# Optimization experiments

Hardware: AMD Instinct MI355X
Metric: run time of the kernel (lower is better)

The kernel has to match this reference:

```python
import jax, jax.numpy as jnp
import numpy as np

ODIM = 8192      # output dim (slice target)
MSIZE = 64       # tile size
N_BLOCKS = 1024  # size of shared block bank


def setup_inputs() -> dict:
    key = jax.random.key(0)
    k1, k2, k3, k4 = jax.random.split(key, 4)
    x = jax.random.normal(k1, (256, 8192), dtype=jnp.float32)
    # bank of msize x msize module blocks (scaled like fan-in init)
    blocks = jax.random.normal(k2, (N_BLOCKS, MSIZE, MSIZE), dtype=jnp.float32) * 0.02
    bound = 1.0 / np.sqrt(ODIM).astype(np.float32)
    bias = jax.random.uniform(k3, (ODIM,), dtype=jnp.float32, minval=-bound, maxval=bound)
    # parts: [icount, ocount] indices into the block bank
    parts = jax.random.randint(k4, (128, 128), 0, N_BLOCKS)
    return {"x": x, "blocks": blocks, "bias": bias, "parts": parts}


def reference(x, blocks, bias, parts):
    icount, ocount = parts.shape
    m = blocks.shape[-1]
    # build_mosaic: gather blocks per parts and tile into a dense weight matrix
    fc = blocks[parts]                                   # [ic, oc, m, m]
    fc_mat = fc.transpose(0, 2, 1, 3).reshape(icount * m, ocount * m)
    # idim (8192) is divisible by msize, so pad is identity (rem == 0 branch)
    y = x @ fc_mat                                       # [B, oc*m]
    y = y[..., :ODIM] + bias                             # slice + bias; post = Identity
    return y
```

## Files before the change

kernel.cpp:

```cpp
#include <hip/hip_runtime.h>
#include <stdint.h>

#define BATCH 256
#define IDIM  8192
#define ODIM  8192
#define MS    64
#define IC    128
#define OC    128
#define NB    1024

#define TM 128
#define TN 128
#define KSPLIT 4
#define NIB (IC / KSPLIT)

#define A_BASE(s) ((s) * 8192)
#define B_BASE(s) (16384 + (s) * 8192)

typedef __bf16 bf16x8 __attribute__((ext_vector_type(8)));
typedef float  floatx4 __attribute__((ext_vector_type(4)));

#define WAITCNT_VM(n) ((((n) & 15) | (((n) >> 4) << 14)) | 0x70 | 0xF00)

__device__ __forceinline__ void async_load16(unsigned short* lds_p, const unsigned short* g_p) {
    __builtin_amdgcn_global_load_lds(
        (const __attribute__((address_space(1))) unsigned int*)g_p,
        (__attribute__((address_space(3))) unsigned int*)lds_p,
        16, 0, 0);
}

__device__ __forceinline__ unsigned short f32_to_bf16(float f) {
    unsigned int u = __float_as_uint(f);
    u += 0x7FFFu + ((u >> 16) & 1u);
    return (unsigned short)(u >> 16);
}

#define XCONV_BLKS 1024
#define PT_BLKS 64
__global__ void k_convert(const float* __restrict__ x, const float* __restrict__ blocks,
                          const int* __restrict__ parts,
                          unsigned short* __restrict__ xb, unsigned short* __restrict__ bt,
                          int* __restrict__ pT) {
    __shared__ float tile[MS][MS + 1];
    int b = blockIdx.x;
    if (b < NB) {
        const float4* src4 = (const float4*)(blocks + (size_t)b * MS * MS);
        unsigned short* dst = bt + (size_t)b * MS * MS;
        #pragma unroll
        for (int i = 0; i < 4; ++i) {
            int slot = i * 256 + threadIdx.x;
            int r = slot >> 4, c4 = (slot & 15) * 4;
            float4 v = src4[slot];
            tile[r][c4 + 0] = v.x; tile[r][c4 + 1] = v.y;
            tile[r][c4 + 2] = v.z; tile[r][c4 + 3] = v.w;
        }
        __syncthreads();
        #pragma unroll
        for (int i = 0; i < 2; ++i) {
            int slot = i * 256 + threadIdx.x;
            int c = slot >> 3, o = slot & 7;
            union { unsigned short s[8]; uint4 v; } u;
            #pragma unroll
            for (int j = 0; j < 8; ++j) u.s[j] = f32_to_bf16(tile[o * 8 + j][c]);
            *(uint4*)(dst + c * MS + o * 8) = u.v;
        }
    } else if (b < NB + XCONV_BLKS) {
        int t = (b - NB) * 256 + threadIdx.x;
        const float4* x4 = (const float4*)x;
        float4 a = x4[2 * t], bb = x4[2 * t + 1];
        union { unsigned short s[8]; uint4 v; } u;
        u.s[0] = f32_to_bf16(a.x);  u.s[1] = f32_to_bf16(a.y);
        u.s[2] = f32_to_bf16(a.z);  u.s[3] = f32_to_bf16(a.w);
        u.s[4] = f32_to_bf16(bb.x); u.s[5] = f32_to_bf16(bb.y);
        u.s[6] = f32_to_bf16(bb.z); u.s[7] = f32_to_bf16(bb.w);
        ((uint4*)xb)[t] = u.v;
    } else {
        int t = (b - NB - XCONV_BLKS) * 256 + threadIdx.x;
        int oc = t >> 7, ic = t & 127;
        pT[t] = parts[ic * OC + oc];
    }
}

extern __shared__ unsigned short smem[];

__global__ __launch_bounds__(256, 2)
void k_mosaic_gemm(const unsigned short* __restrict__ xb,
                   const unsigned short* __restrict__ bt,
                   const int* __restrict__ pT,
                   float* __restrict__ partial) {
    const int tid  = threadIdx.x;
    const int lane = tid & 63;
    const int wave = tid >> 6;
    const int wrow = wave >> 1;
    const int wcol = wave & 1;
    const int nt = blockIdx.x;
    const int mt = blockIdx.y;
    const int ks = blockIdx.z;

    const int m0  = mt * TM;
    const int ob0 = nt * 2;
    const int ib0 = ks * NIB;

    const int row  = lane & 15;
    const int quad = lane >> 4;

    int pv0 = pT[ob0 * IC + ib0 + (lane & 31)];
    int pv1 = pT[(ob0 + 1) * IC + ib0 + (lane & 31)];

    int a_off[2][4], b_off[2][4];
    #pragma unroll
    for (int kk = 0; kk < 2; ++kk) {
        int oct = kk * 4 + quad;
        #pragma unroll
        for (int mi = 0; mi < 4; ++mi) {
            int r = wrow * 64 + mi * 16 + row;
            a_off[kk][mi] = r * MS + ((oct ^ (r & 7)) << 3);
        }
        #pragma unroll
        for (int ni = 0; ni < 4; ++ni) {
            int n = wcol * 64 + ni * 16 + row;
            b_off[kk][ni] = n * MS + ((oct ^ (n & 7)) << 3);
        }
    }

    floatx4 acc[4][4];
    #pragma unroll
    for (int mi = 0; mi < 4; ++mi)
        #pragma unroll
        for (int ni = 0; ni < 4; ++ni)
            acc[mi][ni] = (floatx4){0.f, 0.f, 0.f, 0.f};

#define STAGE_A(abase, ibx) do {                                              \
    _Pragma("unroll")                                                         \
    for (int j = 0; j < 4; ++j) {                                             \
        int slot = j * 256 + tid;               \
        int m = slot >> 3;                                                    \
        int oct = (slot & 7) ^ (m & 7);                                       \
        async_load16(smem + (abase) + slot * 8,                               \
                     xb + (size_t)(m0 + m) * IDIM + (ibx) * MS + oct * 8);    \
    } } while (0)

#define STAGE_B(bbase, pa, pb) do {                                           \
    _Pragma("unroll")                                                         \
    for (int j = 0; j < 4; ++j) {                                             \
        int slot = j * 256 + tid;               \
        int n = slot >> 3;                                                    \
        int oct = (slot & 7) ^ (n & 7);                                       \
        int p = (j < 2) ? (pa) : (pb);                                        \
        async_load16(smem + (bbase) + slot * 8,                               \
                     bt + (size_t)p * (MS * MS) + (n & 63) * MS + oct * 8);   \
    } } while (0)

#define COMPUTE(abase, bbase) do {                                            \
    _Pragma("unroll")                                                         \
    for (int kk = 0; kk < 2; ++kk) {                                          \
        bf16x8 af[4], bfr[4];                                                 \
        _Pragma("unroll")                                                     \
        for (int mi = 0; mi < 4; ++mi)                                        \
            af[mi] = *(const bf16x8*)(smem + (abase) + a_off[kk][mi]);        \
        _Pragma("unroll")                                                     \
        for (int ni = 0; ni < 4; ++ni)                                        \
            bfr[ni] = *(const bf16x8*)(smem + (bbase) + b_off[kk][ni]);       \
        _Pragma("unroll")                                                     \
        for (int mi = 0; mi < 4; ++mi)                                        \
            _Pragma("unroll")                                                 \
            for (int ni = 0; ni < 4; ++ni)                                    \
                acc[mi][ni] = __builtin_amdgcn_mfma_f32_16x16x32_bf16(        \
                    af[mi], bfr[ni], acc[mi][ni], 0, 0, 0);                   \
    } } while (0)

#define ROUND(idx, acS, bcS, asS, bsS) do {                                   \
    STAGE_A(A_BASE(asS), ib0 + (idx) + 1);                                    \
    { int q0 = __shfl(pv0, (idx) + 2), q1 = __shfl(pv1, (idx) + 2);           \
      STAGE_B(B_BASE(bsS), q0, q1); }                                         \
    __builtin_amdgcn_sched_barrier(0);                                        \
    __builtin_amdgcn_s_waitcnt(WAITCNT_VM(12));                               \
    __builtin_amdgcn_s_barrier();                                             \
    __builtin_amdgcn_sched_barrier(0);                                        \
    COMPUTE(A_BASE(acS), B_BASE(bcS));                                        \
    __builtin_amdgcn_sched_barrier(0);                                        \
    __builtin_amdgcn_s_barrier();                                             \
    __builtin_amdgcn_sched_barrier(0);                                        \
    } while (0)

    STAGE_A(A_BASE(0), ib0 + 0);
    { int q0 = __shfl(pv0, 0), q1 = __shfl(pv1, 0); STAGE_B(B_BASE(0), q0, q1); }
    { int q0 = __shfl(pv0, 1), q1 = __shfl(pv1, 1); STAGE_B(B_BASE(1), q0, q1); }

    for (int i6 = 0; i6 < 30; i6 += 6) {
        ROUND(i6 + 0, 0, 0, 1, 2);
        ROUND(i6 + 1, 1, 1, 0, 0);
        ROUND(i6 + 2, 0, 2, 1, 1);
        ROUND(i6 + 3, 1, 0, 0, 2);
        ROUND(i6 + 4, 0, 1, 1, 0);
        ROUND(i6 + 5, 1, 2, 0, 1);
    }
    STAGE_A(A_BASE(1), ib0 + NIB - 1);
    __builtin_amdgcn_sched_barrier(0);
    __builtin_amdgcn_s_waitcnt(WAITCNT_VM(8));
    __builtin_amdgcn_s_barrier();
    __builtin_amdgcn_sched_barrier(0);
    COMPUTE(A_BASE(0), B_BASE(0));
    __builtin_amdgcn_sched_barrier(0);
    __builtin_amdgcn_s_barrier();
    __builtin_amdgcn_sched_barrier(0);
    __builtin_amdgcn_s_waitcnt(WAITCNT_VM(0));
    __builtin_amdgcn_s_barrier();
    __builtin_amdgcn_sched_barrier(0);
    COMPUTE(A_BASE(1), B_BASE(1));

    float* out = partial + (size_t)ks * BATCH * ODIM;
    #pragma unroll
    for (int mi = 0; mi < 4; ++mi)
        #pragma unroll
        for (int ni = 0; ni < 4; ++ni)
            #pragma unroll
            for (int r = 0; r < 4; ++r) {
                int rowg = m0 + wrow * 64 + mi * 16 + quad * 4 + r;
                int colg = nt * TN + wcol * 64 + ni * 16 + row;
                out[(size_t)rowg * ODIM + colg] = acc[mi][ni][r];
            }
}

__global__ void k_reduce_bias(const float* __restrict__ partial,
                              const float* __restrict__ bias,
                              float* __restrict__ out) {
    int t = blockIdx.x * 256 + threadIdx.x;
    const float4* b4 = (const float4*)bias;
    float4 c = b4[t & (ODIM / 4 - 1)];
    float4 r = {c.x, c.y, c.z, c.w};
    #pragma unroll
    for (int k = 0; k < KSPLIT; ++k) {
        const float4* p = (const float4*)(partial + (size_t)k * BATCH * ODIM);
        float4 a = p[t];
        r.x += a.x; r.y += a.y; r.z += a.z; r.w += a.w;
    }
    ((float4*)out)[t] = r;
}

extern "C" void kernel_launch(void* const* d_in, const int* in_sizes, int n_in,
                              void* d_out, int out_size, void* d_ws, size_t ws_size,
                              hipStream_t stream) {
    const float* x      = (const float*)d_in[0];
    const float* blocks = (const float*)d_in[1];
    const float* bias   = (const float*)d_in[2];
    const int*   parts  = (const int*)d_in[3];
    float* out = (float*)d_out;

    char* ws = (char*)d_ws;
    unsigned short* xb      = (unsigned short*)ws;
    unsigned short* btb     = (unsigned short*)(ws + (4u << 20));
    int*            pTr     = (int*)(ws + (12u << 20));
    float*          partial = (float*)(ws + (13u << 20));

    static bool attr_set = false;
    if (!attr_set) {
        hipFuncSetAttribute((const void*)k_mosaic_gemm,
                            hipFuncAttributeMaxDynamicSharedMemorySize, 80 * 1024);
        attr_set = true;
    }

    k_convert<<<NB + XCONV_BLKS + PT_BLKS, 256, 0, stream>>>(x, blocks, parts, xb, btb, pTr);
    k_mosaic_gemm<<<dim3(ODIM / TN, BATCH / TM, KSPLIT), 256, 80 * 1024, stream>>>(xb, btb, pTr, partial);
    k_reduce_bias<<<(BATCH * ODIM) / (256 * 4), 256, 0, stream>>>(partial, bias, out);
}
```

Before: 121.4 us.

## Load A fragments directly from global into double-buffered registers, drop A LDS staging

The A (activation) operand is no longer staged through LDS with async global-to-LDS copies. Each lane now loads its MFMA A fragments straight from global memory into two register banks that alternate across rounds, and only B stays in LDS. This removes A LDS traffic and cuts shared memory from 80KB to 48KB, which may allow more blocks per CU. In exchange it adds 16 vector registers per bank, performs uncoalesced per-lane 16-byte global loads, and changes the waitcnt accounting, which risks stalls or wrong ordering.

```diff
diff --git a/kernel.cpp b/kernel.cpp
--- a/kernel.cpp
+++ b/kernel.cpp
@@ -14,8 +14,7 @@
 #define KSPLIT 4
 #define NIB (IC / KSPLIT)
 
-#define A_BASE(s) ((s) * 8192)
-#define B_BASE(s) (16384 + (s) * 8192)
+#define B_BASE(s) ((s) * 8192)
 
 typedef __bf16 bf16x8 __attribute__((ext_vector_type(8)));
 typedef float  floatx4 __attribute__((ext_vector_type(4)));
@@ -107,15 +106,10 @@
     int pv0 = pT[ob0 * IC + ib0 + (lane & 31)];
     int pv1 = pT[(ob0 + 1) * IC + ib0 + (lane & 31)];
 
-    int a_off[2][4], b_off[2][4];
+    int b_off[2][4];
     #pragma unroll
     for (int kk = 0; kk < 2; ++kk) {
         int oct = kk * 4 + quad;
-        #pragma unroll
-        for (int mi = 0; mi < 4; ++mi) {
-            int r = wrow * 64 + mi * 16 + row;
-            a_off[kk][mi] = r * MS + ((oct ^ (r & 7)) << 3);
-        }
         #pragma unroll
         for (int ni = 0; ni < 4; ++ni) {
             int n = wcol * 64 + ni * 16 + row;
@@ -123,6 +117,8 @@
         }
     }
 
+    const unsigned short* aptr = xb + (size_t)(m0 + wrow * 64 + row) * IDIM + quad * 8;
+
     floatx4 acc[4][4];
     #pragma unroll
     for (int mi = 0; mi < 4; ++mi)
@@ -130,15 +126,16 @@
         for (int ni = 0; ni < 4; ++ni)
             acc[mi][ni] = (floatx4){0.f, 0.f, 0.f, 0.f};
 
-#define STAGE_A(abase, ibx) do {                                              \
+    bf16x8 aA[2][4], aB[2][4];
+
+#define PREFETCH_A(BANK, ibx) do {                                            \
     _Pragma("unroll")                                                         \
-    for (int j = 0; j < 4; ++j) {                                             \
-        int slot = j * 256 + tid;               \
-        int m = slot >> 3;                                                    \
-        int oct = (slot & 7) ^ (m & 7);                                       \
-        async_load16(smem + (abase) + slot * 8,                               \
-                     xb + (size_t)(m0 + m) * IDIM + (ibx) * MS + oct * 8);    \
-    } } while (0)
+    for (int kk = 0; kk < 2; ++kk)                                            \
+        _Pragma("unroll")                                                     \
+        for (int mi = 0; mi < 4; ++mi)                                        \
+            BANK[kk][mi] = *(const bf16x8*)(aptr + (size_t)mi * (16 * IDIM)   \
+                                            + (size_t)(ibx) * MS + kk * 32);  \
+    } while (0)
 
 #define STAGE_B(bbase, pa, pb) do {                                           \
     _Pragma("unroll")                                                         \
@@ -151,13 +148,10 @@
                      bt + (size_t)p * (MS * MS) + (n & 63) * MS + oct * 8);   \
     } } while (0)
 
-#define COMPUTE(abase, bbase) do {                                            \
+#define COMPUTE(BANK, bbase) do {                                             \
     _Pragma("unroll")                                                         \
     for (int kk = 0; kk < 2; ++kk) {                                          \
-        bf16x8 af[4], bfr[4];                                                 \
-        _Pragma("unroll")                                                     \
-        for (int mi = 0; mi < 4; ++mi)                                        \
-            af[mi] = *(const bf16x8*)(smem + (abase) + a_off[kk][mi]);        \
+        bf16x8 bfr[4];                                                        \
         _Pragma("unroll")                                                     \
         for (int ni = 0; ni < 4; ++ni)                                        \
             bfr[ni] = *(const bf16x8*)(smem + (bbase) + b_off[kk][ni]);       \
@@ -166,48 +160,48 @@
             _Pragma("unroll")                                                 \
             for (int ni = 0; ni < 4; ++ni)                                    \
                 acc[mi][ni] = __builtin_amdgcn_mfma_f32_16x16x32_bf16(        \
-                    af[mi], bfr[ni], acc[mi][ni], 0, 0, 0);                   \
+                    BANK[kk][mi], bfr[ni], acc[mi][ni], 0, 0, 0);             \
     } } while (0)
 
-#define ROUND(idx, acS, bcS, asS, bsS) do {                                   \
-    STAGE_A(A_BASE(asS), ib0 + (idx) + 1);                                    \
+#define ROUND(idx, bcS, bsS, BC, BN_, WN) do {                                \
+    PREFETCH_A(BN_, ib0 + (idx) + 1);                                         \
     { int q0 = __shfl(pv0, (idx) + 2), q1 = __shfl(pv1, (idx) + 2);           \
       STAGE_B(B_BASE(bsS), q0, q1); }                                         \
     __builtin_amdgcn_sched_barrier(0);                                        \
-    __builtin_amdgcn_s_waitcnt(WAITCNT_VM(12));                               \
+    __builtin_amdgcn_s_waitcnt(WAITCNT_VM(WN));                               \
     __builtin_amdgcn_s_barrier();                                             \
     __builtin_amdgcn_sched_barrier(0);                                        \
-    COMPUTE(A_BASE(acS), B_BASE(bcS));                                        \
+    COMPUTE(BC, B_BASE(bcS));                                                 \
     __builtin_amdgcn_sched_barrier(0);                                        \
     __builtin_amdgcn_s_barrier();                                             \
     __builtin_amdgcn_sched_barrier(0);                                        \
     } while (0)
 
-    STAGE_A(A_BASE(0), ib0 + 0);
+    PREFETCH_A(aA, ib0 + 0);
     { int q0 = __shfl(pv0, 0), q1 = __shfl(pv1, 0); STAGE_B(B_BASE(0), q0, q1); }
     { int q0 = __shfl(pv0, 1), q1 = __shfl(pv1, 1); STAGE_B(B_BASE(1), q0, q1); }
 
     for (int i6 = 0; i6 < 30; i6 += 6) {
-        ROUND(i6 + 0, 0, 0, 1, 2);
-        ROUND(i6 + 1, 1, 1, 0, 0);
-        ROUND(i6 + 2, 0, 2, 1, 1);
-        ROUND(i6 + 3, 1, 0, 0, 2);
-        ROUND(i6 + 4, 0, 1, 1, 0);
-        ROUND(i6 + 5, 1, 2, 0, 1);
-    }
-    STAGE_A(A_BASE(1), ib0 + NIB - 1);
-    __builtin_amdgcn_sched_barrier(0);
-    __builtin_amdgcn_s_waitcnt(WAITCNT_VM(8));
+        ROUND(i6 + 0, 0, 2, aA, aB, 16);
+        ROUND(i6 + 1, 1, 0, aB, aA, 16);
+        ROUND(i6 + 2, 2, 1, aA, aB, 16);
+        ROUND(i6 + 3, 0, 2, aB, aA, 16);
+        ROUND(i6 + 4, 1, 0, aA, aB, 16);
+        ROUND(i6 + 5, 2, 1, aB, aA, 16);
+    }
+    PREFETCH_A(aB, ib0 + NIB - 1);
+    __builtin_amdgcn_sched_barrier(0);
+    __builtin_amdgcn_s_waitcnt(WAITCNT_VM(12));
     __builtin_amdgcn_s_barrier();
     __builtin_amdgcn_sched_barrier(0);
-    COMPUTE(A_BASE(0), B_BASE(0));
+    COMPUTE(aA, B_BASE(0));
     __builtin_amdgcn_sched_barrier(0);
     __builtin_amdgcn_s_barrier();
     __builtin_amdgcn_sched_barrier(0);
     __builtin_amdgcn_s_waitcnt(WAITCNT_VM(0));
     __builtin_amdgcn_s_barrier();
     __builtin_amdgcn_sched_barrier(0);
-    COMPUTE(A_BASE(1), B_BASE(1));
+    COMPUTE(aB, B_BASE(1));
 
     float* out = partial + (size_t)ks * BATCH * ODIM;
     #pragma unroll
@@ -256,11 +250,11 @@
     static bool attr_set = false;
     if (!attr_set) {
         hipFuncSetAttribute((const void*)k_mosaic_gemm,
-                            hipFuncAttributeMaxDynamicSharedMemorySize, 80 * 1024);
+                            hipFuncAttributeMaxDynamicSharedMemorySize, 48 * 1024);
         attr_set = true;
     }
 
     k_convert<<<NB + XCONV_BLKS + PT_BLKS, 256, 0, stream>>>(x, blocks, parts, xb, btb, pTr);
-    k_mosaic_gemm<<<dim3(ODIM / TN, BATCH / TM, KSPLIT), 256, 80 * 1024, stream>>>(xb, btb, pTr, partial);
+    k_mosaic_gemm<<<dim3(ODIM / TN, BATCH / TM, KSPLIT), 256, 48 * 1024, stream>>>(xb, btb, pTr, partial);
     k_reduce_bias<<<(BATCH * ODIM) / (256 * 4), 256, 0, stream>>>(partial, bias, out);
 }
```

After: 154.2 us. 27.1% more time.
